# Kernel tuning notes

Measured on AMD Instinct MI355X. Metric: run time of the kernel, lower is better.

The kernel has to match this reference:

```python
import jax, jax.numpy as jnp
import numpy as np


def _extract_patches(x):
    # x: [B,28,28] -> [B,196,4]; patch elems [x[r,c], x[r,c+1], x[r+1,c], x[r+1,c+1]]
    B = x.shape[0]
    p = x.reshape(B, 14, 2, 14, 2)           # [B, r, dr, c, dc]
    p = jnp.transpose(p, (0, 1, 3, 2, 4))    # [B, r, c, dr, dc]
    return p.reshape(B, 196, 4)


def _simulate(patches, params):
    # All gates are single-qubit and the state starts at |0000>, so the 4-wire
    # state stays a product state: simulate each qubit as a complex 2-vector
    # (a, b), vectorized over [B, P=196, W=4].
    half = patches * 0.5
    a = jnp.cos(half).astype(jnp.complex64)   # amplitude of |0>
    b = jnp.sin(half).astype(jnp.complex64)   # amplitude of |1>  (RY encoding of |0>)
    depth = params.shape[0]
    for d in range(depth):  # small fixed structural loop
        rz1 = params[d, :, 0]
        ry = params[d, :, 1]
        rz2 = params[d, :, 2]
        # RZ(t) = diag(e^{-it/2}, e^{it/2})
        ph1 = jnp.exp(-0.5j * rz1.astype(jnp.complex64))  # [W], broadcasts over B,P
        a = a * ph1
        b = b * jnp.conj(ph1)
        # RY(t) = [[cos(t/2), -sin(t/2)], [sin(t/2), cos(t/2)]]
        c = jnp.cos(ry * 0.5).astype(jnp.complex64)
        s = jnp.sin(ry * 0.5).astype(jnp.complex64)
        a, b = c * a - s * b, s * a + c * b
        ph2 = jnp.exp(-0.5j * rz2.astype(jnp.complex64))
        a = a * ph2
        b = b * jnp.conj(ph2)
    # <Z> per wire for a product state
    z = (jnp.real(a * jnp.conj(a)) - jnp.real(b * jnp.conj(b))).astype(jnp.float32)  # [B,196,4]
    return z.reshape(z.shape[0], -1)  # [B, 784], patch-major then wire order (matches torch cat)


def setup_inputs() -> dict:
    key = jax.random.key(0)
    k1, k2, k3, k4 = jax.random.split(key, 4)
    B, depth = 8192, 4
    x = jax.random.uniform(k1, (B, 1, 28, 28), dtype=jnp.float32)
    params = jax.random.normal(k2, (depth, 4, 3), dtype=jnp.float32)
    w = jax.random.normal(k3, (10, 784), dtype=jnp.float32) * (1.0 / np.sqrt(784.0))
    bias = jax.random.normal(k4, (10,), dtype=jnp.float32) * 0.01
    return {"x": x, "params": params, "w": w, "bias": bias}


def reference(x, params, w, bias):
    B = x.shape[0]
    patches = _extract_patches(x.reshape(B, 28, 28))
    feats = _simulate(patches, params)          # [B, 784]
    logits = feats @ w.T + bias                 # [B, 10]
    return jax.nn.log_softmax(logits, axis=-1)
```

## Files before the change

### kernel.cpp

```cpp
#include <hip/hip_runtime.h>
#include <math.h>

#define NCH 256

struct c2 { float re, im; };
__device__ inline c2 cmul(c2 a, c2 b){ return {a.re*b.re - a.im*b.im, a.re*b.im + a.im*b.re}; }
__device__ inline c2 cadd(c2 a, c2 b){ return {a.re+b.re, a.im+b.im}; }

__device__ inline void su2_alpha_beta(const float* __restrict__ params, float* Aq, float* Bq) {
    #pragma unroll
    for (int q = 0; q < 4; ++q) {
        c2 m00 = {1.f, 0.f}, m01 = {0.f, 0.f}, m10 = {0.f, 0.f}, m11 = {1.f, 0.f};
        #pragma unroll
        for (int d = 0; d < 4; ++d) {
            float rz1 = params[(d * 4 + q) * 3 + 0];
            float ry  = params[(d * 4 + q) * 3 + 1];
            float rz2 = params[(d * 4 + q) * 3 + 2];
            float c  = __cosf(0.5f * ry),  s  = __sinf(0.5f * ry);
            c2 ph1  = { __cosf(0.5f * rz1), -__sinf(0.5f * rz1) };
            c2 ph1c = { ph1.re, -ph1.im };
            c2 ph2  = { __cosf(0.5f * rz2), -__sinf(0.5f * rz2) };
            c2 ph2c = { ph2.re, -ph2.im };
            c2 d00 = cmul(ph2,  { c * ph1.re,  c * ph1.im });
            c2 d01 = cmul(ph2,  {-s * ph1c.re, -s * ph1c.im});
            c2 d10 = cmul(ph2c, { s * ph1.re,  s * ph1.im });
            c2 d11 = cmul(ph2c, { c * ph1c.re, c * ph1c.im});
            c2 n00 = cadd(cmul(d00, m00), cmul(d01, m10));
            c2 n01 = cadd(cmul(d00, m01), cmul(d01, m11));
            c2 n10 = cadd(cmul(d10, m00), cmul(d11, m10));
            c2 n11 = cadd(cmul(d10, m01), cmul(d11, m11));
            m00 = n00; m01 = n01; m10 = n10; m11 = n11;
        }
        float n00 = m00.re*m00.re + m00.im*m00.im;
        float n10 = m10.re*m10.re + m10.im*m10.im;
        float n01 = m01.re*m01.re + m01.im*m01.im;
        float n11 = m11.re*m11.re + m11.im*m11.im;
        Aq[q] = 0.5f * (n00 - n10 - n01 + n11);
        Bq[q] = (m00.re*m01.re + m00.im*m01.im) - (m10.re*m11.re + m10.im*m11.im);
    }
}

__global__ __launch_bounds__(256) void k0_table(
    const float* __restrict__ params, const float* __restrict__ w,
    float4* __restrict__ tab4)
{
    int slot = blockIdx.x;
    int c    = threadIdx.x;
    float Aq[4], Bq[4];
    if (slot < 2) su2_alpha_beta(params, Aq, Bq);
    float v[4];
    #pragma unroll
    for (int e = 0; e < 4; ++e) {
        int m = c * 4 + e;
        float val = 0.f;
        if (m < 784) {
            int r = m / 28, col = m - 28 * r;
            int q = ((r & 1) << 1) | (col & 1);
            if (slot == 0)      val = Aq[q];
            else if (slot == 1) val = Bq[q];
            else {
                int f = ((r >> 1) * 14 + (col >> 1)) * 4 + q;
                val = w[(slot - 2) * 784 + f];
            }
        }
        v[e] = val;
    }
    tab4[slot * NCH + c] = make_float4(v[0], v[1], v[2], v[3]);
}

__global__ __launch_bounds__(256) void k_main(
    const float* __restrict__ x, const float4* __restrict__ tab4,
    const float* __restrict__ bias, float* __restrict__ out, int Bn)
{
    __shared__ __align__(16) float4 lds4[12 * NCH];
    __shared__ float wls[4][40];

    const int tid  = threadIdx.x;
    const int lane = tid & 63;
    const int wid  = tid >> 6;

    #pragma unroll
    for (int k = 0; k < 12; ++k) lds4[tid + 256 * k] = tab4[tid + 256 * k];
    __syncthreads();

    const float4* x4 = (const float4*)x;
    int b0 = blockIdx.x * 16 + wid * 4;
    size_t xb[4];
    #pragma unroll
    for (int s = 0; s < 4; ++s) {
        int bs = b0 + s; if (bs > Bn - 1) bs = Bn - 1;
        xb[s] = (size_t)bs * 196;
    }

    float acc[4][10];
    #pragma unroll
    for (int s = 0; s < 4; ++s)
        #pragma unroll
        for (int cl = 0; cl < 10; ++cl) acc[s][cl] = 0.f;

    #pragma unroll
    for (int it = 0; it < 4; ++it) {
        int c  = it * 64 + lane;
        int cx = c < 196 ? c : 195;
        float4 xv[4];
        #pragma unroll
        for (int s = 0; s < 4; ++s) xv[s] = x4[xb[s] + cx];
        float4 al = lds4[c];
        float4 be = lds4[NCH + c];
        float z[4][4];
        #pragma unroll
        for (int s = 0; s < 4; ++s) {
            z[s][0] = fmaf(al.x, __cosf(xv[s].x), be.x * __sinf(xv[s].x));
            z[s][1] = fmaf(al.y, __cosf(xv[s].y), be.y * __sinf(xv[s].y));
            z[s][2] = fmaf(al.z, __cosf(xv[s].z), be.z * __sinf(xv[s].z));
            z[s][3] = fmaf(al.w, __cosf(xv[s].w), be.w * __sinf(xv[s].w));
        }
        #pragma unroll
        for (int cl = 0; cl < 10; ++cl) {
            float4 wv = lds4[(2 + cl) * NCH + c];
            #pragma unroll
            for (int s = 0; s < 4; ++s) {
                acc[s][cl] = fmaf(z[s][0], wv.x, acc[s][cl]);
                acc[s][cl] = fmaf(z[s][1], wv.y, acc[s][cl]);
                acc[s][cl] = fmaf(z[s][2], wv.z, acc[s][cl]);
                acc[s][cl] = fmaf(z[s][3], wv.w, acc[s][cl]);
            }
        }
    }

    #pragma unroll
    for (int s = 0; s < 4; ++s) {
        #pragma unroll
        for (int cl = 0; cl < 10; ++cl) {
            float v = acc[s][cl];
            v += __shfl_xor(v, 32, 64);
            v += __shfl_xor(v, 16, 64);
            v += __shfl_xor(v,  8, 64);
            v += __shfl_xor(v,  4, 64);
            v += __shfl_xor(v,  2, 64);
            v += __shfl_xor(v,  1, 64);
            if (lane == 0) wls[wid][s * 10 + cl] = v;
        }
    }
    __syncthreads();

    if (lane < 40) {
        int s = lane / 10, cl = lane - 10 * s;
        const float* L = &wls[wid][s * 10];
        float mx = -1e30f;
        #pragma unroll
        for (int k = 0; k < 10; ++k) { float v = L[k] + bias[k]; mx = fmaxf(mx, v); }
        float sum = 0.f;
        #pragma unroll
        for (int k = 0; k < 10; ++k) sum += __expf(L[k] + bias[k] - mx);
        float lse = mx + __logf(sum);
        int b = b0 + s;
        if (b < Bn) out[b * 10 + cl] = (L[cl] + bias[cl]) - lse;
    }
}

extern "C" void kernel_launch(void* const* d_in, const int* in_sizes, int n_in,
                              void* d_out, int out_size, void* d_ws, size_t ws_size,
                              hipStream_t stream) {
    const float* x      = (const float*)d_in[0];
    const float* params = (const float*)d_in[1];
    const float* w      = (const float*)d_in[2];
    const float* bias   = (const float*)d_in[3];
    float* out = (float*)d_out;
    int Bn = in_sizes[0] / 784;

    float4* tab4 = (float4*)d_ws;

    k0_table<<<12, 256, 0, stream>>>(params, w, tab4);
    k_main<<<(Bn + 15) / 16, 256, 0, stream>>>(x, tab4, bias, out, Bn);
}
```

Before: 97.21 us.

## Fuse table-precompute kernel into main kernel, building LDS tables per block

Removes the separate table-building kernel and its global workspace round trip. Each block now computes the per-qubit alpha/beta coefficients itself and scatters the weight matrix into the permuted shared-memory layout directly from global memory. This saves one kernel launch and the dependency between the two kernels. In exchange, every block redoes the small SU(2) product and the weight gather, which adds per-block prologue latency.

```diff
diff --git a/kernel.cpp b/kernel.cpp
--- a/kernel.cpp
+++ b/kernel.cpp
@@ -40,47 +40,53 @@
     }
 }
 
-__global__ __launch_bounds__(256) void k0_table(
-    const float* __restrict__ params, const float* __restrict__ w,
-    float4* __restrict__ tab4)
+__global__ __launch_bounds__(256) void quanv_one(
+    const float* __restrict__ x, const float* __restrict__ params,
+    const float* __restrict__ w, const float* __restrict__ bias,
+    float* __restrict__ out, int Bn)
 {
-    int slot = blockIdx.x;
-    int c    = threadIdx.x;
-    float Aq[4], Bq[4];
-    if (slot < 2) su2_alpha_beta(params, Aq, Bq);
-    float v[4];
-    #pragma unroll
-    for (int e = 0; e < 4; ++e) {
-        int m = c * 4 + e;
-        float val = 0.f;
-        if (m < 784) {
-            int r = m / 28, col = m - 28 * r;
-            int q = ((r & 1) << 1) | (col & 1);
-            if (slot == 0)      val = Aq[q];
-            else if (slot == 1) val = Bq[q];
-            else {
-                int f = ((r >> 1) * 14 + (col >> 1)) * 4 + q;
-                val = w[(slot - 2) * 784 + f];
-            }
-        }
-        v[e] = val;
-    }
-    tab4[slot * NCH + c] = make_float4(v[0], v[1], v[2], v[3]);
-}
-
-__global__ __launch_bounds__(256) void k_main(
-    const float* __restrict__ x, const float4* __restrict__ tab4,
-    const float* __restrict__ bias, float* __restrict__ out, int Bn)
-{
-    __shared__ __align__(16) float4 lds4[12 * NCH];
+    __shared__ __align__(16) float tab[12 * 1024];
     __shared__ float wls[4][40];
 
     const int tid  = threadIdx.x;
     const int lane = tid & 63;
     const int wid  = tid >> 6;
 
-    #pragma unroll
-    for (int k = 0; k < 12; ++k) lds4[tid + 256 * k] = tab4[tid + 256 * k];
+    float Aq[4], Bq[4];
+    su2_alpha_beta(params, Aq, Bq);
+
+    float4* tab4 = (float4*)tab;
+    {
+        int c = tid;
+        if (c < 196) {
+            int rp = (c / 7) & 1;
+            float a0 = Aq[2 * rp], a1 = Aq[2 * rp + 1];
+            float b0 = Bq[2 * rp], b1 = Bq[2 * rp + 1];
+            tab4[c]       = make_float4(a0, a1, a0, a1);
+            tab4[NCH + c] = make_float4(b0, b1, b0, b1);
+        } else {
+            tab4[c]       = make_float4(0.f, 0.f, 0.f, 0.f);
+            tab4[NCH + c] = make_float4(0.f, 0.f, 0.f, 0.f);
+            #pragma unroll
+            for (int sl = 2; sl < 12; ++sl)
+                tab4[sl * NCH + c] = make_float4(0.f, 0.f, 0.f, 0.f);
+        }
+    }
+    {
+        const float4* w4 = (const float4*)w;
+        #pragma unroll
+        for (int k = 0; k < 8; ++k) {
+            int idx4 = tid + 256 * k;
+            if (idx4 < 1960) {
+                float4 v = w4[idx4];
+                int cl = idx4 / 196, p = idx4 - 196 * cl;
+                int pi = p / 14, pj = p - 14 * pi;
+                int base = (2 + cl) * 1024 + 56 * pi + 2 * pj;
+                *(float2*)&tab[base]      = make_float2(v.x, v.y);
+                *(float2*)&tab[base + 28] = make_float2(v.z, v.w);
+            }
+        }
+    }
     __syncthreads();
 
     const float4* x4 = (const float4*)x;
@@ -105,8 +111,8 @@
         float4 xv[4];
         #pragma unroll
         for (int s = 0; s < 4; ++s) xv[s] = x4[xb[s] + cx];
-        float4 al = lds4[c];
-        float4 be = lds4[NCH + c];
+        float4 al = tab4[c];
+        float4 be = tab4[NCH + c];
         float z[4][4];
         #pragma unroll
         for (int s = 0; s < 4; ++s) {
@@ -117,7 +123,7 @@
         }
         #pragma unroll
         for (int cl = 0; cl < 10; ++cl) {
-            float4 wv = lds4[(2 + cl) * NCH + c];
+            float4 wv = tab4[(2 + cl) * NCH + c];
             #pragma unroll
             for (int s = 0; s < 4; ++s) {
                 acc[s][cl] = fmaf(z[s][0], wv.x, acc[s][cl]);
@@ -168,9 +174,5 @@
     const float* bias   = (const float*)d_in[3];
     float* out = (float*)d_out;
     int Bn = in_sizes[0] / 784;
-
-    float4* tab4 = (float4*)d_ws;
-
-    k0_table<<<12, 256, 0, stream>>>(params, w, tab4);
-    k_main<<<(Bn + 15) / 16, 256, 0, stream>>>(x, tab4, bias, out, Bn);
+    quanv_one<<<(Bn + 15) / 16, 256, 0, stream>>>(x, params, w, bias, out, Bn);
 }
```

Measured after the change: 99.77 us. 1.03x slower.
